# Performance work log

Hardware: AMD Instinct MI355X
Metric: run time of the kernel (lower is better)

The kernel has to match this reference:

```python
import jax, jax.numpy as jnp
import numpy as np

B, S, D, U = 32, 2048, 1024, 1024


def setup_inputs() -> dict:
    key = jax.random.key(0)
    ks = jax.random.split(key, 10)
    s = 0.02
    return {
        "dec_hidden": jax.random.normal(ks[0], (B, D), jnp.float32),
        "enc_output": jax.random.normal(ks[1], (B, S, D), jnp.float32),
        "enc_pad_mask": jnp.ones((B, S), jnp.int32),  # accepted but unused, as in the original
        "use_coverage": True,
        "prev_coverage": jax.random.uniform(ks[2], (B, S, 1), jnp.float32),
        "Ws_w": jax.random.normal(ks[3], (D, U), jnp.float32) * s,
        "Ws_b": jnp.zeros((U,), jnp.float32),
        "Wh_w": jax.random.normal(ks[4], (D, U), jnp.float32) * s,
        "Wh_b": jnp.zeros((U,), jnp.float32),
        "Wc_w": jax.random.normal(ks[5], (1, U), jnp.float32) * s,
        "Wc_b": jnp.zeros((U,), jnp.float32),
        "V_w": jax.random.normal(ks[6], (U, 1), jnp.float32) * s,
        "V_b": jnp.zeros((1,), jnp.float32),
    }


def reference(dec_hidden, enc_output, enc_pad_mask, use_coverage, prev_coverage,
              Ws_w, Ws_b, Wh_w, Wh_b, Wc_w, Wc_b, V_w, V_b):
    # W_h(dec_hidden) with time axis: [B, 1, U]
    h = (dec_hidden @ Wh_w + Wh_b)[:, None, :]
    # W_s(enc_output): [B, S, U]
    feat = jnp.einsum('bsd,du->bsu', enc_output, Ws_w) + Ws_b + h
    if use_coverage and prev_coverage is not None:
        # W_c(prev_coverage): [B, S, 1] @ [1, U] -> [B, S, U]
        feat = feat + prev_coverage @ Wc_w + Wc_b
        score = jnp.tanh(feat) @ V_w + V_b            # [B, S, 1]
        attention_weights = jax.nn.softmax(score, axis=1)
        coverage = attention_weights + prev_coverage
    else:
        score = jnp.tanh(feat) @ V_w + V_b
        attention_weights = jax.nn.softmax(score, axis=1)
        coverage = attention_weights if use_coverage else []
    # weighted sum over sequence axis: [B, D]
    context_vector = jnp.sum(attention_weights * enc_output, axis=1)
    return context_vector, jnp.squeeze(attention_weights, -1), coverage
```

## Files before the change

kernel.cpp:

```cpp
#include <hip/hip_runtime.h>
#include <hip/hip_bf16.h>

namespace {

constexpr int kB = 32;
constexpr int kS = 2048;
constexpr int kD = 1024;
constexpr int kU = 1024;
constexpr int BM = 128;
constexpr int BN = 128;
constexpr int BK = 64;
constexpr int kMT = (kB * kS) / BM;
constexpr int kNT = kU / BN;
constexpr int kKS = kD / BK;
constexpr size_t kChunk = (size_t)BM * BK * 2;

typedef __attribute__((ext_vector_type(8))) short bf16x8;
typedef __attribute__((ext_vector_type(4))) float f32x4;

__device__ __forceinline__ unsigned short f2bf(float x) {
  union { __hip_bfloat16 h; unsigned short u; } c;
  c.h = __float2bfloat16(x);
  return c.u;
}

__device__ __forceinline__ float tanh_fast(float x) {
  float e = __expf(2.0f * x);
  return 1.0f - 2.0f * __builtin_amdgcn_rcpf(e + 1.0f);
}

__device__ __forceinline__ void gload16(const void* g, void* l) {
  __builtin_amdgcn_global_load_lds(
      (const __attribute__((address_space(1))) void*)g,
      (__attribute__((address_space(3))) void*)l, 16, 0, 0);
}


__global__ __launch_bounds__(256) void h2_kernel(
    const float* __restrict__ dec, const float* __restrict__ Whw,
    const float* __restrict__ Whb, const float* __restrict__ Wsb,
    const float* __restrict__ Wcb, float* __restrict__ h2) {
  const int b = blockIdx.y;
  const int u = blockIdx.x * 256 + threadIdx.x;
  float acc = Whb[u] + Wsb[u] + Wcb[u];
  const float* dh = dec + b * kD;
  #pragma unroll 8
  for (int d = 0; d < kD; ++d) acc += dh[d] * Whw[(size_t)d * kU + u];
  h2[b * kU + u] = acc;
}

__global__ __launch_bounds__(256) void context_kernel(
    const float* __restrict__ enc, const float* __restrict__ attn,
    float* __restrict__ ctx) {
  const int b = blockIdx.z;
  const int s0 = blockIdx.y * 256;
  const int d = blockIdx.x * 256 + threadIdx.x;
  const float* e = enc + ((size_t)b * kS + s0) * kD + d;
  const float* a = attn + (size_t)b * kS + s0;
  float acc = 0.f;
  #pragma unroll 8
  for (int s = 0; s < 256; ++s) acc += a[s] * e[(size_t)s * kD];
  atomicAdd(&ctx[b * kD + d], acc);
}


__global__ __launch_bounds__(256) void convA_kernel(
    const float* __restrict__ enc, unsigned char* __restrict__ encT) {
  const size_t e = ((size_t)blockIdx.x * 256 + threadIdx.x) * 8;
  const int r = (int)(e >> 10), d0 = (int)(e & 1023);
  float4 v0 = *(const float4*)(enc + e);
  float4 v1 = *(const float4*)(enc + e + 4);
  uint4 p;
  p.x = (unsigned)f2bf(v0.x) | ((unsigned)f2bf(v0.y) << 16);
  p.y = (unsigned)f2bf(v0.z) | ((unsigned)f2bf(v0.w) << 16);
  p.z = (unsigned)f2bf(v1.x) | ((unsigned)f2bf(v1.y) << 16);
  p.w = (unsigned)f2bf(v1.z) | ((unsigned)f2bf(v1.w) << 16);
  const int mt = r >> 7, row = r & 127, ks = d0 >> 6, c = d0 & 63;
  unsigned char* dst = encT + ((size_t)mt * kKS + ks) * kChunk + row * 128 +
                       (((c >> 3) << 4) ^ ((row & 7) << 4));
  *(uint4*)dst = p;
}

__global__ __launch_bounds__(256) void tpose2_kernel(
    const float* __restrict__ W, unsigned char* __restrict__ Bt) {
  __shared__ float tile[32][33];
  const int u0 = blockIdx.x * 32, d0 = blockIdx.y * 32;
  const int tx = threadIdx.x, ty = threadIdx.y;
  #pragma unroll
  for (int i = 0; i < 4; ++i)
    tile[ty + i * 8][tx] = W[(size_t)(d0 + ty + i * 8) * kU + u0 + tx];
  __syncthreads();
  #pragma unroll
  for (int i = 0; i < 4; ++i) {
    const int u = u0 + ty + i * 8, d = d0 + tx;
    const int nt = u >> 7, n = u & 127, ks = d >> 6, c = d & 63;
    *(unsigned short*)(Bt + ((size_t)nt * kKS + ks) * kChunk + n * 128 +
                       ((((c >> 3) << 4) ^ ((n & 7) << 4)) + (c & 7) * 2)) =
        f2bf(tile[tx][ty + i * 8]);
  }
}

__global__ __launch_bounds__(256, 4) void score_gemm2_kernel(
    const unsigned char* __restrict__ encT, const unsigned char* __restrict__ Bt,
    const float* __restrict__ h2, const float* __restrict__ pc,
    const float* __restrict__ Wcw, const float* __restrict__ Vw,
    float* __restrict__ scorep) {
  __shared__ __attribute__((aligned(16))) unsigned char smA[kChunk];
  __shared__ __attribute__((aligned(16))) unsigned char smB[kChunk];

  const int tid = threadIdx.x;
  const int lane = tid & 63;
  const int w = tid >> 6;
  const int wr = w >> 1, wc = w & 1;

  const int work = (blockIdx.x & 7) * (kMT * kNT / 8) + (blockIdx.x >> 3);
  const int mtile = work >> 3, ntile = work & 7;
  const int r0 = mtile * BM, n0 = ntile * BN;

  const unsigned char* Ab = encT + (size_t)mtile * kKS * kChunk + (size_t)w * 4096 + lane * 16;
  const unsigned char* Bb = Bt + (size_t)ntile * kKS * kChunk + (size_t)w * 4096 + lane * 16;

  f32x4 acc[4][4];
  #pragma unroll
  for (int i = 0; i < 4; ++i)
    #pragma unroll
    for (int j = 0; j < 4; ++j) acc[i][j] = (f32x4){0.f, 0.f, 0.f, 0.f};

  const int lr = lane & 15, lq = lane >> 4;

  for (int ks = 0; ks < kKS; ++ks) {
    #pragma unroll
    for (int i = 0; i < 4; ++i) {
      gload16(Ab + (size_t)ks * kChunk + i * 1024, smA + w * 4096 + i * 1024);
      gload16(Bb + (size_t)ks * kChunk + i * 1024, smB + w * 4096 + i * 1024);
    }
    __syncthreads();
    #pragma unroll
    for (int k2 = 0; k2 < 2; ++k2) {
      const int kb = k2 * 64 + lq * 16;
      bf16x8 af[4], bfr[4];
      #pragma unroll
      for (int fm = 0; fm < 4; ++fm) {
        const int row = wr * 64 + fm * 16 + lr;
        af[fm] = *(const bf16x8*)(smA + row * 128 + (kb ^ ((row & 7) << 4)));
      }
      #pragma unroll
      for (int fn = 0; fn < 4; ++fn) {
        const int n = wc * 64 + fn * 16 + lr;
        bfr[fn] = *(const bf16x8*)(smB + n * 128 + (kb ^ ((n & 7) << 4)));
      }
      #pragma unroll
      for (int fm = 0; fm < 4; ++fm)
        #pragma unroll
        for (int fn = 0; fn < 4; ++fn)
          acc[fm][fn] =
              __builtin_amdgcn_mfma_f32_16x16x32_bf16(af[fm], bfr[fn], acc[fm][fn], 0, 0, 0);
    }
    __syncthreads();
  }

  const int bidx = r0 >> 11;
  float hv[4], wv[4], vv[4];
  #pragma unroll
  for (int fn = 0; fn < 4; ++fn) {
    const int u = n0 + wc * 64 + fn * 16 + lr;
    hv[fn] = h2[bidx * kU + u];
    wv[fn] = Wcw[u];
    vv[fn] = Vw[u];
  }
  float* plane = scorep + (size_t)((ntile << 1) | wc) * (kB * kS);
  #pragma unroll
  for (int fm = 0; fm < 4; ++fm) {
    #pragma unroll
    for (int j = 0; j < 4; ++j) {
      const int r = r0 + wr * 64 + fm * 16 + lq * 4 + j;
      const float pcv = pc[r];
      float partial = 0.f;
      #pragma unroll
      for (int fn = 0; fn < 4; ++fn) {
        const float feat = acc[fm][fn][j] + hv[fn] + pcv * wv[fn];
        partial += tanh_fast(feat) * vv[fn];
      }
      partial += __shfl_xor(partial, 1);
      partial += __shfl_xor(partial, 2);
      partial += __shfl_xor(partial, 4);
      partial += __shfl_xor(partial, 8);
      if (lr == 0) plane[r] = partial;
    }
  }
}

__global__ __launch_bounds__(256) void softmax2_kernel(
    const float* __restrict__ scorep, const float* __restrict__ pc,
    float* __restrict__ attn, float* __restrict__ cov) {
  const int b = blockIdx.x, tid = threadIdx.x;
  const int lane = tid & 63, wid = tid >> 6;
  const size_t base = (size_t)b * kS + tid * 8;
  float v[8] = {0.f, 0.f, 0.f, 0.f, 0.f, 0.f, 0.f, 0.f};
  #pragma unroll
  for (int p = 0; p < 16; ++p) {
    const float* s = scorep + (size_t)p * (kB * kS) + base;
    float4 a = *(const float4*)(s);
    float4 c = *(const float4*)(s + 4);
    v[0] += a.x; v[1] += a.y; v[2] += a.z; v[3] += a.w;
    v[4] += c.x; v[5] += c.y; v[6] += c.z; v[7] += c.w;
  }
  float m = v[0];
  #pragma unroll
  for (int i = 1; i < 8; ++i) m = fmaxf(m, v[i]);
  #pragma unroll
  for (int msk = 1; msk < 64; msk <<= 1) m = fmaxf(m, __shfl_xor(m, msk));
  __shared__ float redm[4], reds[4];
  if (lane == 0) redm[wid] = m;
  __syncthreads();
  m = fmaxf(fmaxf(redm[0], redm[1]), fmaxf(redm[2], redm[3]));
  float e[8], sum = 0.f;
  #pragma unroll
  for (int i = 0; i < 8; ++i) { e[i] = __expf(v[i] - m); sum += e[i]; }
  #pragma unroll
  for (int msk = 1; msk < 64; msk <<= 1) sum += __shfl_xor(sum, msk);
  if (lane == 0) reds[wid] = sum;
  __syncthreads();
  sum = reds[0] + reds[1] + reds[2] + reds[3];
  const float inv = 1.0f / sum;
  float pv[8], a[8], c[8];
  const float* p = pc + base;
  *(float4*)(pv) = *(const float4*)(p);
  *(float4*)(pv + 4) = *(const float4*)(p + 4);
  #pragma unroll
  for (int i = 0; i < 8; ++i) { a[i] = e[i] * inv; c[i] = a[i] + pv[i]; }
  *(float4*)(attn + base) = *(float4*)(a);
  *(float4*)(attn + base + 4) = *(float4*)(a + 4);
  *(float4*)(cov + base) = *(float4*)(c);
  *(float4*)(cov + base + 4) = *(float4*)(c + 4);
}


__global__ __launch_bounds__(256) void tpose_fb_kernel(
    const float* __restrict__ W, unsigned short* __restrict__ out) {
  __shared__ float tile[32][33];
  const int u0 = blockIdx.x * 32, d0 = blockIdx.y * 32;
  const int tx = threadIdx.x, ty = threadIdx.y;
  #pragma unroll
  for (int i = 0; i < 4; ++i)
    tile[ty + i * 8][tx] = W[(size_t)(d0 + ty + i * 8) * kU + u0 + tx];
  __syncthreads();
  #pragma unroll
  for (int i = 0; i < 4; ++i)
    out[(size_t)(u0 + ty + i * 8) * kD + d0 + tx] = f2bf(tile[tx][ty + i * 8]);
}

__global__ __launch_bounds__(256, 2) void score_gemm_fb_kernel(
    const float* __restrict__ enc, const unsigned short* __restrict__ WsT,
    const float* __restrict__ h2, const float* __restrict__ pc,
    const float* __restrict__ Wcw, const float* __restrict__ Vw,
    float* __restrict__ score) {
  __shared__ __attribute__((aligned(16))) unsigned char smA[BM * BK * 2];
  __shared__ __attribute__((aligned(16))) unsigned char smB[BN * BK * 2];
  const int tid = threadIdx.x;
  const int lane = tid & 63;
  const int wid = tid >> 6;
  const int wr = wid >> 1, wc = wid & 1;
  const int mtile = blockIdx.x >> 3, ntile = blockIdx.x & 7;
  const int r0 = mtile * BM, n0 = ntile * BN;
  f32x4 acc[4][4];
  #pragma unroll
  for (int i = 0; i < 4; ++i)
    #pragma unroll
    for (int j = 0; j < 4; ++j) acc[i][j] = (f32x4){0.f, 0.f, 0.f, 0.f};
  const int kqA = tid & 15;
  const int rowA = tid >> 4;
  const int kcB = tid & 7;
  const int nB = tid >> 3;
  float4 aReg[8];
  uint4 bReg[4];
  #pragma unroll
  for (int i = 0; i < 8; ++i)
    aReg[i] = *(const float4*)(enc + (size_t)(r0 + rowA + 16 * i) * kD + kqA * 4);
  #pragma unroll
  for (int i = 0; i < 4; ++i)
    bReg[i] = *(const uint4*)(WsT + (size_t)(n0 + nB + 32 * i) * kD + kcB * 8);
  const int lr = lane & 15, lq = lane >> 4;
  for (int k0 = 0; k0 < kD; k0 += BK) {
    #pragma unroll
    for (int i = 0; i < 8; ++i) {
      const int row = rowA + 16 * i;
      uint2 p;
      p.x = (unsigned)f2bf(aReg[i].x) | ((unsigned)f2bf(aReg[i].y) << 16);
      p.y = (unsigned)f2bf(aReg[i].z) | ((unsigned)f2bf(aReg[i].w) << 16);
      *(uint2*)(smA + row * 128 + ((kqA * 8) ^ ((row & 7) << 4))) = p;
    }
    #pragma unroll
    for (int i = 0; i < 4; ++i) {
      const int n = nB + 32 * i;
      *(uint4*)(smB + n * 128 + ((kcB * 16) ^ ((n & 7) << 4))) = bReg[i];
    }
    __syncthreads();
    if (k0 + BK < kD) {
      const int kn = k0 + BK;
      #pragma unroll
      for (int i = 0; i < 8; ++i)
        aReg[i] = *(const float4*)(enc + (size_t)(r0 + rowA + 16 * i) * kD + kn + kqA * 4);
      #pragma unroll
      for (int i = 0; i < 4; ++i)
        bReg[i] = *(const uint4*)(WsT + (size_t)(n0 + nB + 32 * i) * kD + kn + kcB * 8);
    }
    #pragma unroll
    for (int ks = 0; ks < 2; ++ks) {
      const int kb = ks * 64 + lq * 16;
      bf16x8 af[4], bfr[4];
      #pragma unroll
      for (int fm = 0; fm < 4; ++fm) {
        const int row = wr * 64 + fm * 16 + lr;
        af[fm] = *(const bf16x8*)(smA + row * 128 + (kb ^ ((row & 7) << 4)));
      }
      #pragma unroll
      for (int fn = 0; fn < 4; ++fn) {
        const int n = wc * 64 + fn * 16 + lr;
        bfr[fn] = *(const bf16x8*)(smB + n * 128 + (kb ^ ((n & 7) << 4)));
      }
      #pragma unroll
      for (int fm = 0; fm < 4; ++fm)
        #pragma unroll
        for (int fn = 0; fn < 4; ++fn)
          acc[fm][fn] =
              __builtin_amdgcn_mfma_f32_16x16x32_bf16(af[fm], bfr[fn], acc[fm][fn], 0, 0, 0);
    }
    __syncthreads();
  }
  const int bidx = r0 >> 11;
  float hv[4], wv[4], vv[4];
  #pragma unroll
  for (int fn = 0; fn < 4; ++fn) {
    const int u = n0 + wc * 64 + fn * 16 + lr;
    hv[fn] = h2[bidx * kU + u];
    wv[fn] = Wcw[u];
    vv[fn] = Vw[u];
  }
  #pragma unroll
  for (int fm = 0; fm < 4; ++fm) {
    #pragma unroll
    for (int j = 0; j < 4; ++j) {
      const int r = r0 + wr * 64 + fm * 16 + lq * 4 + j;
      const float pcv = pc[r];
      float partial = 0.f;
      #pragma unroll
      for (int fn = 0; fn < 4; ++fn) {
        const float feat = acc[fm][fn][j] + hv[fn] + pcv * wv[fn];
        partial += tanh_fast(feat) * vv[fn];
      }
      partial += __shfl_xor(partial, 1);
      partial += __shfl_xor(partial, 2);
      partial += __shfl_xor(partial, 4);
      partial += __shfl_xor(partial, 8);
      if (lr == 0) atomicAdd(&score[r], partial);
    }
  }
}

__global__ __launch_bounds__(256) void softmax_fb_kernel(
    const float* __restrict__ score, const float* __restrict__ pc,
    float* __restrict__ attn, float* __restrict__ cov) {
  const int b = blockIdx.x, tid = threadIdx.x;
  const int lane = tid & 63, wid = tid >> 6;
  const float* s = score + (size_t)b * kS;
  float v[8];
  *(float4*)(v) = *(const float4*)(s + tid * 8);
  *(float4*)(v + 4) = *(const float4*)(s + tid * 8 + 4);
  float m = v[0];
  #pragma unroll
  for (int i = 1; i < 8; ++i) m = fmaxf(m, v[i]);
  #pragma unroll
  for (int msk = 1; msk < 64; msk <<= 1) m = fmaxf(m, __shfl_xor(m, msk));
  __shared__ float redm[4], reds[4];
  if (lane == 0) redm[wid] = m;
  __syncthreads();
  m = fmaxf(fmaxf(redm[0], redm[1]), fmaxf(redm[2], redm[3]));
  float e[8], sum = 0.f;
  #pragma unroll
  for (int i = 0; i < 8; ++i) { e[i] = __expf(v[i] - m); sum += e[i]; }
  #pragma unroll
  for (int msk = 1; msk < 64; msk <<= 1) sum += __shfl_xor(sum, msk);
  if (lane == 0) reds[wid] = sum;
  __syncthreads();
  sum = reds[0] + reds[1] + reds[2] + reds[3];
  const float inv = 1.0f / sum;
  float pv[8], a[8], c[8];
  const float* p = pc + (size_t)b * kS + tid * 8;
  *(float4*)(pv) = *(const float4*)(p);
  *(float4*)(pv + 4) = *(const float4*)(p + 4);
  #pragma unroll
  for (int i = 0; i < 8; ++i) { a[i] = e[i] * inv; c[i] = a[i] + pv[i]; }
  *(float4*)(attn + (size_t)b * kS + tid * 8) = *(float4*)(a);
  *(float4*)(attn + (size_t)b * kS + tid * 8 + 4) = *(float4*)(a + 4);
  *(float4*)(cov + (size_t)b * kS + tid * 8) = *(float4*)(c);
  *(float4*)(cov + (size_t)b * kS + tid * 8 + 4) = *(float4*)(c + 4);
}

}

extern "C" void kernel_launch(void* const* d_in, const int* in_sizes, int n_in,
                              void* d_out, int out_size, void* d_ws, size_t ws_size,
                              hipStream_t stream) {
  (void)in_sizes; (void)n_in; (void)out_size;
  const float* dec = (const float*)d_in[0];
  const float* enc = (const float*)d_in[1];
  const float* pc  = (const float*)d_in[4];
  const float* Wsw = (const float*)d_in[5];
  const float* Wsb = (const float*)d_in[6];
  const float* Whw = (const float*)d_in[7];
  const float* Whb = (const float*)d_in[8];
  const float* Wcw = (const float*)d_in[9];
  const float* Wcb = (const float*)d_in[10];
  const float* Vw  = (const float*)d_in[11];

  float* ctx  = (float*)d_out;
  float* attn = (float*)d_out + kB * kD;
  float* cov  = attn + kB * kS;

  unsigned char* ws = (unsigned char*)d_ws;

  const size_t encT_sz  = (size_t)kB * kS * kD * 2;
  const size_t Bt_sz    = (size_t)kU * kD * 2;
  const size_t h2_sz    = (size_t)kB * kU * 4;
  const size_t sp_sz    = (size_t)16 * kB * kS * 4;
  const size_t need     = encT_sz + Bt_sz + h2_sz + sp_sz;

  hipMemsetAsync(ctx, 0, kB * kD * sizeof(float), stream);

  if (ws_size >= need) {
    unsigned char* encT = ws;
    unsigned char* Bt   = ws + encT_sz;
    float* h2     = (float*)(ws + encT_sz + Bt_sz);
    float* scorep = (float*)(ws + encT_sz + Bt_sz + h2_sz);

    convA_kernel<<<dim3((kB * kS * kD / 8) / 256), 256, 0, stream>>>(enc, encT);
    tpose2_kernel<<<dim3(kU / 32, kD / 32), dim3(32, 8), 0, stream>>>(Wsw, Bt);
    h2_kernel<<<dim3(kU / 256, kB), 256, 0, stream>>>(dec, Whw, Whb, Wsb, Wcb, h2);
    score_gemm2_kernel<<<dim3(kMT * kNT), 256, 0, stream>>>(
        encT, Bt, h2, pc, Wcw, Vw, scorep);
    softmax2_kernel<<<dim3(kB), 256, 0, stream>>>(scorep, pc, attn, cov);
    context_kernel<<<dim3(kD / 256, kS / 256, kB), 256, 0, stream>>>(enc, attn, ctx);
  } else {
    unsigned short* WsT = (unsigned short*)ws;
    float* h2    = (float*)(ws + (size_t)2 * 1024 * 1024);
    float* score = (float*)(ws + (size_t)2 * 1024 * 1024 + 131072);
    hipMemsetAsync(score, 0, kB * kS * sizeof(float), stream);
    h2_kernel<<<dim3(kU / 256, kB), 256, 0, stream>>>(dec, Whw, Whb, Wsb, Wcb, h2);
    tpose_fb_kernel<<<dim3(kU / 32, kD / 32), dim3(32, 8), 0, stream>>>(Wsw, WsT);
    score_gemm_fb_kernel<<<dim3(kMT * kNT), 256, 0, stream>>>(
        enc, WsT, h2, pc, Wcw, Vw, score);
    softmax_fb_kernel<<<dim3(kB), 256, 0, stream>>>(score, pc, attn, cov);
    context_kernel<<<dim3(kD / 256, kS / 256, kB), 256, 0, stream>>>(enc, attn, ctx);
  }
}
```

Baseline: 347.0 us.

## Fuse prep kernels and compute context from bf16 encoder copy

```diff
diff --git a/kernel.cpp b/kernel.cpp
--- a/kernel.cpp
+++ b/kernel.cpp
@@ -7,13 +7,16 @@
 constexpr int kS = 2048;
 constexpr int kD = 1024;
 constexpr int kU = 1024;
-constexpr int BM = 128;
-constexpr int BN = 128;
-constexpr int BK = 64;
-constexpr int kMT = (kB * kS) / BM;
-constexpr int kNT = kU / BN;
-constexpr int kKS = kD / BK;
-constexpr size_t kChunk = (size_t)BM * BK * 2;
+
+constexpr int kKT = kD / 64;
+constexpr size_t kHalf = 16384;
+constexpr size_t kTileChunk = 2 * kHalf;
+constexpr size_t kPanel = (size_t)kKT * kTileChunk;
+
+constexpr int kConvBlocks = (kB * kS * kD / 8) / 256;
+constexpr int kTpBlocks = (kU / 32) * (kD / 32);
+constexpr int kH2Blocks = (kU / 64) * (kB / 4);
+constexpr int kPrepBlocks = kConvBlocks + kTpBlocks + kH2Blocks;
 
 typedef __attribute__((ext_vector_type(8))) short bf16x8;
 typedef __attribute__((ext_vector_type(4))) float f32x4;
@@ -24,6 +27,12 @@
   return c.u;
 }
 
+__device__ __forceinline__ float bf2f(unsigned short u) {
+  union { unsigned int i; float f; } c;
+  c.i = ((unsigned int)u) << 16;
+  return c.f;
+}
+
 __device__ __forceinline__ float tanh_fast(float x) {
   float e = __expf(2.0f * x);
   return 1.0f - 2.0f * __builtin_amdgcn_rcpf(e + 1.0f);
@@ -35,21 +44,419 @@
       (__attribute__((address_space(3))) void*)l, 16, 0, 0);
 }
 
-
-__global__ __launch_bounds__(256) void h2_kernel(
+#define MFMA_BF16(a, b, c) __builtin_amdgcn_mfma_f32_16x16x32_bf16((a), (b), (c), 0, 0, 0)
+
+
+__global__ __launch_bounds__(256) void prep_kernel(
+    const float* __restrict__ enc, unsigned char* __restrict__ encT,
+    const float* __restrict__ Wsw, unsigned char* __restrict__ Bt,
     const float* __restrict__ dec, const float* __restrict__ Whw,
     const float* __restrict__ Whb, const float* __restrict__ Wsb,
     const float* __restrict__ Wcb, float* __restrict__ h2) {
+  __shared__ float tile[32][33];
+  const int bid = blockIdx.x;
+  if (bid < kConvBlocks) {
+    const size_t e = ((size_t)bid * 256 + threadIdx.x) * 8;
+    const int r = (int)(e >> 10), d0 = (int)(e & 1023);
+    float4 v0 = *(const float4*)(enc + e);
+    float4 v1 = *(const float4*)(enc + e + 4);
+    uint4 p;
+    p.x = (unsigned)f2bf(v0.x) | ((unsigned)f2bf(v0.y) << 16);
+    p.y = (unsigned)f2bf(v0.z) | ((unsigned)f2bf(v0.w) << 16);
+    p.z = (unsigned)f2bf(v1.x) | ((unsigned)f2bf(v1.y) << 16);
+    p.w = (unsigned)f2bf(v1.z) | ((unsigned)f2bf(v1.w) << 16);
+    const int mt = r >> 8, rh = (r >> 7) & 1, row = r & 127;
+    const int kt = d0 >> 6, c8 = (d0 & 63) >> 3;
+    unsigned char* dst = encT + (size_t)mt * kPanel + (size_t)kt * kTileChunk +
+                         (size_t)rh * kHalf + row * 128 +
+                         (((unsigned)c8 << 4) ^ (((unsigned)row & 7) << 4));
+    *(uint4*)dst = p;
+  } else if (bid < kConvBlocks + kTpBlocks) {
+    const int q = bid - kConvBlocks;
+    const int u0 = (q & 31) * 32, d0 = (q >> 5) * 32;
+    const int tx = threadIdx.x & 31, ty = threadIdx.x >> 5;
+    #pragma unroll
+    for (int i = 0; i < 4; ++i)
+      tile[ty + i * 8][tx] = Wsw[(size_t)(d0 + ty + i * 8) * kU + u0 + tx];
+    __syncthreads();
+    #pragma unroll
+    for (int i = 0; i < 4; ++i) {
+      const int u = u0 + ty + i * 8, d = d0 + tx;
+      const int nt = u >> 8, gh = (u >> 7) & 1, n = u & 127;
+      const int kt = d >> 6, c = d & 63;
+      *(unsigned short*)(Bt + (size_t)nt * kPanel + (size_t)kt * kTileChunk +
+                         (size_t)gh * kHalf + n * 128 +
+                         (((((unsigned)c >> 3) << 4) ^ (((unsigned)n & 7) << 4)) +
+                          (c & 7) * 2)) = f2bf(tile[tx][ty + i * 8]);
+    }
+  } else {
+    const int q = bid - kConvBlocks - kTpBlocks;
+    const int u = (q & 15) * 64 + (threadIdx.x & 63);
+    const int b = (q >> 4) * 4 + (threadIdx.x >> 6);
+    float acc = 0.f;
+    const float* dh = dec + b * kD;
+    #pragma unroll 8
+    for (int d = 0; d < kD; ++d) acc += dh[d] * Whw[(size_t)d * kU + u];
+    h2[b * kU + u] = acc + Whb[u] + Wsb[u] + Wcb[u];
+  }
+}
+
+__global__ __launch_bounds__(256, 8) void score_gemm6_kernel(
+    const unsigned char* __restrict__ encT, const unsigned char* __restrict__ Bt,
+    const float* __restrict__ h2, const float* __restrict__ pc,
+    const float* __restrict__ Wcw, const float* __restrict__ Vw,
+    float* __restrict__ scorep) {
+  __shared__ __attribute__((aligned(16))) unsigned char smA[16384];
+  __shared__ __attribute__((aligned(16))) unsigned char smB[16384];
+
+  const int tid = threadIdx.x;
+  const int lane = tid & 63;
+  const int w = tid >> 6;
+  const int wr = w >> 1, wc = w & 1;
+  const int work = (blockIdx.x & 7) * 512 + (blockIdx.x >> 3);
+  const int mtile = work >> 3, ntile = work & 7;
+  const int r0 = mtile * 128, n0 = ntile * 128;
+
+  const unsigned char* Ab = encT + (size_t)(mtile >> 1) * kPanel +
+                            (size_t)(mtile & 1) * kHalf + (size_t)w * 4096 + lane * 16;
+  const unsigned char* Bb = Bt + (size_t)(ntile >> 1) * kPanel +
+                            (size_t)(ntile & 1) * kHalf + (size_t)w * 4096 + lane * 16;
+
+  f32x4 acc[4][4];
+  #pragma unroll
+  for (int i = 0; i < 4; ++i)
+    #pragma unroll
+    for (int j = 0; j < 4; ++j) acc[i][j] = (f32x4){0.f, 0.f, 0.f, 0.f};
+
+  const int lr = lane & 15, lq = lane >> 4;
+
+  for (int ks = 0; ks < kKT; ++ks) {
+    #pragma unroll
+    for (int i = 0; i < 4; ++i) {
+      gload16(Ab + (size_t)ks * kTileChunk + i * 1024, smA + w * 4096 + i * 1024);
+      gload16(Bb + (size_t)ks * kTileChunk + i * 1024, smB + w * 4096 + i * 1024);
+    }
+    __syncthreads();
+    #pragma unroll
+    for (int k2 = 0; k2 < 2; ++k2) {
+      const int kb = k2 * 64 + lq * 16;
+      bf16x8 af[4], bfr[4];
+      #pragma unroll
+      for (int fm = 0; fm < 4; ++fm) {
+        const int row = wr * 64 + fm * 16 + lr;
+        af[fm] = *(const bf16x8*)(smA + row * 128 + (kb ^ ((row & 7) << 4)));
+      }
+      #pragma unroll
+      for (int fn = 0; fn < 4; ++fn) {
+        const int n = wc * 64 + fn * 16 + lr;
+        bfr[fn] = *(const bf16x8*)(smB + n * 128 + (kb ^ ((n & 7) << 4)));
+      }
+      #pragma unroll
+      for (int fm = 0; fm < 4; ++fm)
+        #pragma unroll
+        for (int fn = 0; fn < 4; ++fn)
+          acc[fm][fn] = MFMA_BF16(af[fm], bfr[fn], acc[fm][fn]);
+    }
+    __syncthreads();
+  }
+
+  const int bidx = r0 >> 11;
+  float hv[4], wv[4], vv[4];
+  #pragma unroll
+  for (int fn = 0; fn < 4; ++fn) {
+    const int u = n0 + wc * 64 + fn * 16 + lr;
+    hv[fn] = h2[bidx * kU + u];
+    wv[fn] = Wcw[u];
+    vv[fn] = Vw[u];
+  }
+  float* plane = scorep + (size_t)((ntile << 1) | wc) * (kB * kS);
+  #pragma unroll
+  for (int fm = 0; fm < 4; ++fm) {
+    #pragma unroll
+    for (int j = 0; j < 4; ++j) {
+      const int r = r0 + wr * 64 + fm * 16 + lq * 4 + j;
+      const float pcv = pc[r];
+      float partial = 0.f;
+      #pragma unroll
+      for (int fn = 0; fn < 4; ++fn) {
+        const float feat = acc[fm][fn][j] + hv[fn] + pcv * wv[fn];
+        partial += tanh_fast(feat) * vv[fn];
+      }
+      partial += __shfl_xor(partial, 1);
+      partial += __shfl_xor(partial, 2);
+      partial += __shfl_xor(partial, 4);
+      partial += __shfl_xor(partial, 8);
+      if (lr == 0) plane[r] = partial;
+    }
+  }
+}
+
+__global__ __launch_bounds__(256) void softmax2_kernel(
+    const float* __restrict__ scorep, const float* __restrict__ pc,
+    float* __restrict__ attn, float* __restrict__ cov) {
+  const int b = blockIdx.x, tid = threadIdx.x;
+  const int lane = tid & 63, wid = tid >> 6;
+  const size_t base = (size_t)b * kS + tid * 8;
+  float v[8] = {0.f, 0.f, 0.f, 0.f, 0.f, 0.f, 0.f, 0.f};
+  #pragma unroll
+  for (int p = 0; p < 16; ++p) {
+    const float* s = scorep + (size_t)p * (kB * kS) + base;
+    float4 a = *(const float4*)(s);
+    float4 c = *(const float4*)(s + 4);
+    v[0] += a.x; v[1] += a.y; v[2] += a.z; v[3] += a.w;
+    v[4] += c.x; v[5] += c.y; v[6] += c.z; v[7] += c.w;
+  }
+  float m = v[0];
+  #pragma unroll
+  for (int i = 1; i < 8; ++i) m = fmaxf(m, v[i]);
+  #pragma unroll
+  for (int msk = 1; msk < 64; msk <<= 1) m = fmaxf(m, __shfl_xor(m, msk));
+  __shared__ float redm[4], reds[4];
+  if (lane == 0) redm[wid] = m;
+  __syncthreads();
+  m = fmaxf(fmaxf(redm[0], redm[1]), fmaxf(redm[2], redm[3]));
+  float e[8], sum = 0.f;
+  #pragma unroll
+  for (int i = 0; i < 8; ++i) { e[i] = __expf(v[i] - m); sum += e[i]; }
+  #pragma unroll
+  for (int msk = 1; msk < 64; msk <<= 1) sum += __shfl_xor(sum, msk);
+  if (lane == 0) reds[wid] = sum;
+  __syncthreads();
+  sum = reds[0] + reds[1] + reds[2] + reds[3];
+  const float inv = 1.0f / sum;
+  float pv[8], a[8], c[8];
+  const float* p = pc + base;
+  *(float4*)(pv) = *(const float4*)(p);
+  *(float4*)(pv + 4) = *(const float4*)(p + 4);
+  #pragma unroll
+  for (int i = 0; i < 8; ++i) { a[i] = e[i] * inv; c[i] = a[i] + pv[i]; }
+  *(float4*)(attn + base) = *(float4*)(a);
+  *(float4*)(attn + base + 4) = *(float4*)(a + 4);
+  *(float4*)(cov + base) = *(float4*)(c);
+  *(float4*)(cov + base + 4) = *(float4*)(c + 4);
+}
+
+__global__ __launch_bounds__(256) void context2_kernel(
+    const unsigned char* __restrict__ encT, const float* __restrict__ attn,
+    float* __restrict__ ctx) {
+  const int kt = blockIdx.x;
   const int b = blockIdx.y;
-  const int u = blockIdx.x * 256 + threadIdx.x;
-  float acc = Whb[u] + Wsb[u] + Wcb[u];
+  const int cg = threadIdx.x & 7;
+  const int rgrp = threadIdx.x >> 3;
+  float acc8[8];
+  #pragma unroll
+  for (int j = 0; j < 8; ++j) acc8[j] = 0.f;
+  const float* ab = attn + (size_t)b * kS;
+  for (int it = 0; it < kS / 32; ++it) {
+    const int s = it * 32 + rgrp;
+    const int r = b * kS + s;
+    const int mt = r >> 8, rh = (r >> 7) & 1, row = r & 127;
+    const unsigned char* chunk = encT + (size_t)mt * kPanel +
+                                 (size_t)kt * kTileChunk + (size_t)rh * kHalf;
+    uint4 v = *(const uint4*)(chunk + row * 128 +
+                              ((((unsigned)cg << 4) ^ (((unsigned)row & 7) << 4))));
+    const float a = ab[s];
+    const unsigned int* vw = (const unsigned int*)&v;
+    #pragma unroll
+    for (int q = 0; q < 4; ++q) {
+      acc8[2 * q]     += a * bf2f((unsigned short)(vw[q] & 0xffff));
+      acc8[2 * q + 1] += a * bf2f((unsigned short)(vw[q] >> 16));
+    }
+  }
+  __shared__ float red[256 * 8];
+  #pragma unroll
+  for (int j = 0; j < 8; ++j) red[threadIdx.x * 8 + j] = acc8[j];
+  __syncthreads();
+  for (int stride = 16; stride > 0; stride >>= 1) {
+    if (rgrp < stride) {
+      #pragma unroll
+      for (int j = 0; j < 8; ++j)
+        red[(rgrp * 8 + cg) * 8 + j] += red[((rgrp + stride) * 8 + cg) * 8 + j];
+    }
+    __syncthreads();
+  }
+  if (rgrp == 0) {
+    #pragma unroll
+    for (int j = 0; j < 8; ++j)
+      ctx[(size_t)b * kD + kt * 64 + cg * 8 + j] = red[cg * 8 + j];
+  }
+}
+
+
+__global__ __launch_bounds__(256) void h2b_kernel(
+    const float* __restrict__ dec, const float* __restrict__ Whw,
+    const float* __restrict__ Whb, const float* __restrict__ Wsb,
+    const float* __restrict__ Wcb, float* __restrict__ h2) {
+  const int u = blockIdx.x * 64 + (threadIdx.x & 63);
+  const int b = blockIdx.y * 4 + (threadIdx.x >> 6);
+  float acc = 0.f;
   const float* dh = dec + b * kD;
   #pragma unroll 8
   for (int d = 0; d < kD; ++d) acc += dh[d] * Whw[(size_t)d * kU + u];
-  h2[b * kU + u] = acc;
-}
-
-__global__ __launch_bounds__(256) void context_kernel(
+  h2[b * kU + u] = acc + Whb[u] + Wsb[u] + Wcb[u];
+}
+
+__global__ __launch_bounds__(256) void tpose_fb_kernel(
+    const float* __restrict__ W, unsigned short* __restrict__ out) {
+  __shared__ float tile[32][33];
+  const int u0 = blockIdx.x * 32, d0 = blockIdx.y * 32;
+  const int tx = threadIdx.x & 31, ty = threadIdx.x >> 5;
+  #pragma unroll
+  for (int i = 0; i < 4; ++i)
+    tile[ty + i * 8][tx] = W[(size_t)(d0 + ty + i * 8) * kU + u0 + tx];
+  __syncthreads();
+  #pragma unroll
+  for (int i = 0; i < 4; ++i)
+    out[(size_t)(u0 + ty + i * 8) * kD + d0 + tx] = f2bf(tile[tx][ty + i * 8]);
+}
+
+__global__ __launch_bounds__(256, 2) void score_gemm_fb_kernel(
+    const float* __restrict__ enc, const unsigned short* __restrict__ WsT,
+    const float* __restrict__ h2, const float* __restrict__ pc,
+    const float* __restrict__ Wcw, const float* __restrict__ Vw,
+    float* __restrict__ score) {
+  __shared__ __attribute__((aligned(16))) unsigned char smA[128 * 64 * 2];
+  __shared__ __attribute__((aligned(16))) unsigned char smB[128 * 64 * 2];
+  const int tid = threadIdx.x;
+  const int lane = tid & 63;
+  const int wid = tid >> 6;
+  const int wr = wid >> 1, wc = wid & 1;
+  const int mtile = blockIdx.x >> 3, ntile = blockIdx.x & 7;
+  const int r0 = mtile * 128, n0 = ntile * 128;
+  f32x4 acc[4][4];
+  #pragma unroll
+  for (int i = 0; i < 4; ++i)
+    #pragma unroll
+    for (int j = 0; j < 4; ++j) acc[i][j] = (f32x4){0.f, 0.f, 0.f, 0.f};
+  const int kqA = tid & 15;
+  const int rowA = tid >> 4;
+  const int kcB = tid & 7;
+  const int nB = tid >> 3;
+  float4 aReg[8];
+  uint4 bReg[4];
+  #pragma unroll
+  for (int i = 0; i < 8; ++i)
+    aReg[i] = *(const float4*)(enc + (size_t)(r0 + rowA + 16 * i) * kD + kqA * 4);
+  #pragma unroll
+  for (int i = 0; i < 4; ++i)
+    bReg[i] = *(const uint4*)(WsT + (size_t)(n0 + nB + 32 * i) * kD + kcB * 8);
+  const int lr = lane & 15, lq = lane >> 4;
+  for (int k0 = 0; k0 < kD; k0 += 64) {
+    #pragma unroll
+    for (int i = 0; i < 8; ++i) {
+      const int row = rowA + 16 * i;
+      uint2 p;
+      p.x = (unsigned)f2bf(aReg[i].x) | ((unsigned)f2bf(aReg[i].y) << 16);
+      p.y = (unsigned)f2bf(aReg[i].z) | ((unsigned)f2bf(aReg[i].w) << 16);
+      *(uint2*)(smA + row * 128 + ((kqA * 8) ^ ((row & 7) << 4))) = p;
+    }
+    #pragma unroll
+    for (int i = 0; i < 4; ++i) {
+      const int n = nB + 32 * i;
+      *(uint4*)(smB + n * 128 + ((kcB * 16) ^ ((n & 7) << 4))) = bReg[i];
+    }
+    __syncthreads();
+    if (k0 + 64 < kD) {
+      const int kn = k0 + 64;
+      #pragma unroll
+      for (int i = 0; i < 8; ++i)
+        aReg[i] = *(const float4*)(enc + (size_t)(r0 + rowA + 16 * i) * kD + kn + kqA * 4);
+      #pragma unroll
+      for (int i = 0; i < 4; ++i)
+        bReg[i] = *(const uint4*)(WsT + (size_t)(n0 + nB + 32 * i) * kD + kn + kcB * 8);
+    }
+    #pragma unroll
+    for (int ks = 0; ks < 2; ++ks) {
+      const int kb = ks * 64 + lq * 16;
+      bf16x8 af2[4], bfr[4];
+      #pragma unroll
+      for (int fm = 0; fm < 4; ++fm) {
+        const int row = wr * 64 + fm * 16 + lr;
+        af2[fm] = *(const bf16x8*)(smA + row * 128 + (kb ^ ((row & 7) << 4)));
+      }
+      #pragma unroll
+      for (int fn = 0; fn < 4; ++fn) {
+        const int n = wc * 64 + fn * 16 + lr;
+        bfr[fn] = *(const bf16x8*)(smB + n * 128 + (kb ^ ((n & 7) << 4)));
+      }
+      #pragma unroll
+      for (int fm = 0; fm < 4; ++fm)
+        #pragma unroll
+        for (int fn = 0; fn < 4; ++fn)
+          acc[fm][fn] = MFMA_BF16(af2[fm], bfr[fn], acc[fm][fn]);
+    }
+    __syncthreads();
+  }
+  const int bidx = r0 >> 11;
+  float hv[4], wv[4], vv[4];
+  #pragma unroll
+  for (int fn = 0; fn < 4; ++fn) {
+    const int u = n0 + wc * 64 + fn * 16 + lr;
+    hv[fn] = h2[bidx * kU + u];
+    wv[fn] = Wcw[u];
+    vv[fn] = Vw[u];
+  }
+  #pragma unroll
+  for (int fm = 0; fm < 4; ++fm) {
+    #pragma unroll
+    for (int j = 0; j < 4; ++j) {
+      const int r = r0 + wr * 64 + fm * 16 + lq * 4 + j;
+      const float pcv = pc[r];
+      float partial = 0.f;
+      #pragma unroll
+      for (int fn = 0; fn < 4; ++fn) {
+        const float feat = acc[fm][fn][j] + hv[fn] + pcv * wv[fn];
+        partial += tanh_fast(feat) * vv[fn];
+      }
+      partial += __shfl_xor(partial, 1);
+      partial += __shfl_xor(partial, 2);
+      partial += __shfl_xor(partial, 4);
+      partial += __shfl_xor(partial, 8);
+      if (lr == 0) atomicAdd(&score[r], partial);
+    }
+  }
+}
+
+__global__ __launch_bounds__(256) void softmax_fb_kernel(
+    const float* __restrict__ score, const float* __restrict__ pc,
+    float* __restrict__ attn, float* __restrict__ cov) {
+  const int b = blockIdx.x, tid = threadIdx.x;
+  const int lane = tid & 63, wid = tid >> 6;
+  const float* s = score + (size_t)b * kS;
+  float v[8];
+  *(float4*)(v) = *(const float4*)(s + tid * 8);
+  *(float4*)(v + 4) = *(const float4*)(s + tid * 8 + 4);
+  float m = v[0];
+  #pragma unroll
+  for (int i = 1; i < 8; ++i) m = fmaxf(m, v[i]);
+  #pragma unroll
+  for (int msk = 1; msk < 64; msk <<= 1) m = fmaxf(m, __shfl_xor(m, msk));
+  __shared__ float redm[4], reds[4];
+  if (lane == 0) redm[wid] = m;
+  __syncthreads();
+  m = fmaxf(fmaxf(redm[0], redm[1]), fmaxf(redm[2], redm[3]));
+  float e[8], sum = 0.f;
+  #pragma unroll
+  for (int i = 0; i < 8; ++i) { e[i] = __expf(v[i] - m); sum += e[i]; }
+  #pragma unroll
+  for (int msk = 1; msk < 64; msk <<= 1) sum += __shfl_xor(sum, msk);
+  if (lane == 0) reds[wid] = sum;
+  __syncthreads();
+  sum = reds[0] + reds[1] + reds[2] + reds[3];
+  const float inv = 1.0f / sum;
+  float pv[8], a[8], c[8];
+  const float* p = pc + (size_t)b * kS + tid * 8;
+  *(float4*)(pv) = *(const float4*)(p);
+  *(float4*)(pv + 4) = *(const float4*)(p + 4);
+  #pragma unroll
+  for (int i = 0; i < 8; ++i) { a[i] = e[i] * inv; c[i] = a[i] + pv[i]; }
+  *(float4*)(attn + (size_t)b * kS + tid * 8) = *(float4*)(a);
+  *(float4*)(attn + (size_t)b * kS + tid * 8 + 4) = *(float4*)(a + 4);
+  *(float4*)(cov + (size_t)b * kS + tid * 8) = *(float4*)(c);
+  *(float4*)(cov + (size_t)b * kS + tid * 8 + 4) = *(float4*)(c + 4);
+}
+
+__global__ __launch_bounds__(256) void context_fb_kernel(
     const float* __restrict__ enc, const float* __restrict__ attn,
     float* __restrict__ ctx) {
   const int b = blockIdx.z;
@@ -61,340 +468,6 @@
   #pragma unroll 8
   for (int s = 0; s < 256; ++s) acc += a[s] * e[(size_t)s * kD];
   atomicAdd(&ctx[b * kD + d], acc);
-}
-
-
-__global__ __launch_bounds__(256) void convA_kernel(
-    const float* __restrict__ enc, unsigned char* __restrict__ encT) {
-  const size_t e = ((size_t)blockIdx.x * 256 + threadIdx.x) * 8;
-  const int r = (int)(e >> 10), d0 = (int)(e & 1023);
-  float4 v0 = *(const float4*)(enc + e);
-  float4 v1 = *(const float4*)(enc + e + 4);
-  uint4 p;
-  p.x = (unsigned)f2bf(v0.x) | ((unsigned)f2bf(v0.y) << 16);
-  p.y = (unsigned)f2bf(v0.z) | ((unsigned)f2bf(v0.w) << 16);
-  p.z = (unsigned)f2bf(v1.x) | ((unsigned)f2bf(v1.y) << 16);
-  p.w = (unsigned)f2bf(v1.z) | ((unsigned)f2bf(v1.w) << 16);
-  const int mt = r >> 7, row = r & 127, ks = d0 >> 6, c = d0 & 63;
-  unsigned char* dst = encT + ((size_t)mt * kKS + ks) * kChunk + row * 128 +
-                       (((c >> 3) << 4) ^ ((row & 7) << 4));
-  *(uint4*)dst = p;
-}
-
-__global__ __launch_bounds__(256) void tpose2_kernel(
-    const float* __restrict__ W, unsigned char* __restrict__ Bt) {
-  __shared__ float tile[32][33];
-  const int u0 = blockIdx.x * 32, d0 = blockIdx.y * 32;
-  const int tx = threadIdx.x, ty = threadIdx.y;
-  #pragma unroll
-  for (int i = 0; i < 4; ++i)
-    tile[ty + i * 8][tx] = W[(size_t)(d0 + ty + i * 8) * kU + u0 + tx];
-  __syncthreads();
-  #pragma unroll
-  for (int i = 0; i < 4; ++i) {
-    const int u = u0 + ty + i * 8, d = d0 + tx;
-    const int nt = u >> 7, n = u & 127, ks = d >> 6, c = d & 63;
-    *(unsigned short*)(Bt + ((size_t)nt * kKS + ks) * kChunk + n * 128 +
-                       ((((c >> 3) << 4) ^ ((n & 7) << 4)) + (c & 7) * 2)) =
-        f2bf(tile[tx][ty + i * 8]);
-  }
-}
-
-__global__ __launch_bounds__(256, 4) void score_gemm2_kernel(
-    const unsigned char* __restrict__ encT, const unsigned char* __restrict__ Bt,
-    const float* __restrict__ h2, const float* __restrict__ pc,
-    const float* __restrict__ Wcw, const float* __restrict__ Vw,
-    float* __restrict__ scorep) {
-  __shared__ __attribute__((aligned(16))) unsigned char smA[kChunk];
-  __shared__ __attribute__((aligned(16))) unsigned char smB[kChunk];
-
-  const int tid = threadIdx.x;
-  const int lane = tid & 63;
-  const int w = tid >> 6;
-  const int wr = w >> 1, wc = w & 1;
-
-  const int work = (blockIdx.x & 7) * (kMT * kNT / 8) + (blockIdx.x >> 3);
-  const int mtile = work >> 3, ntile = work & 7;
-  const int r0 = mtile * BM, n0 = ntile * BN;
-
-  const unsigned char* Ab = encT + (size_t)mtile * kKS * kChunk + (size_t)w * 4096 + lane * 16;
-  const unsigned char* Bb = Bt + (size_t)ntile * kKS * kChunk + (size_t)w * 4096 + lane * 16;
-
-  f32x4 acc[4][4];
-  #pragma unroll
-  for (int i = 0; i < 4; ++i)
-    #pragma unroll
-    for (int j = 0; j < 4; ++j) acc[i][j] = (f32x4){0.f, 0.f, 0.f, 0.f};
-
-  const int lr = lane & 15, lq = lane >> 4;
-
-  for (int ks = 0; ks < kKS; ++ks) {
-    #pragma unroll
-    for (int i = 0; i < 4; ++i) {
-      gload16(Ab + (size_t)ks * kChunk + i * 1024, smA + w * 4096 + i * 1024);
-      gload16(Bb + (size_t)ks * kChunk + i * 1024, smB + w * 4096 + i * 1024);
-    }
-    __syncthreads();
-    #pragma unroll
-    for (int k2 = 0; k2 < 2; ++k2) {
-      const int kb = k2 * 64 + lq * 16;
-      bf16x8 af[4], bfr[4];
-      #pragma unroll
-      for (int fm = 0; fm < 4; ++fm) {
-        const int row = wr * 64 + fm * 16 + lr;
-        af[fm] = *(const bf16x8*)(smA + row * 128 + (kb ^ ((row & 7) << 4)));
-      }
-      #pragma unroll
-      for (int fn = 0; fn < 4; ++fn) {
-        const int n = wc * 64 + fn * 16 + lr;
-        bfr[fn] = *(const bf16x8*)(smB + n * 128 + (kb ^ ((n & 7) << 4)));
-      }
-      #pragma unroll
-      for (int fm = 0; fm < 4; ++fm)
-        #pragma unroll
-        for (int fn = 0; fn < 4; ++fn)
-          acc[fm][fn] =
-              __builtin_amdgcn_mfma_f32_16x16x32_bf16(af[fm], bfr[fn], acc[fm][fn], 0, 0, 0);
-    }
-    __syncthreads();
-  }
-
-  const int bidx = r0 >> 11;
-  float hv[4], wv[4], vv[4];
-  #pragma unroll
-  for (int fn = 0; fn < 4; ++fn) {
-    const int u = n0 + wc * 64 + fn * 16 + lr;
-    hv[fn] = h2[bidx * kU + u];
-    wv[fn] = Wcw[u];
-    vv[fn] = Vw[u];
-  }
-  float* plane = scorep + (size_t)((ntile << 1) | wc) * (kB * kS);
-  #pragma unroll
-  for (int fm = 0; fm < 4; ++fm) {
-    #pragma unroll
-    for (int j = 0; j < 4; ++j) {
-      const int r = r0 + wr * 64 + fm * 16 + lq * 4 + j;
-      const float pcv = pc[r];
-      float partial = 0.f;
-      #pragma unroll
-      for (int fn = 0; fn < 4; ++fn) {
-        const float feat = acc[fm][fn][j] + hv[fn] + pcv * wv[fn];
-        partial += tanh_fast(feat) * vv[fn];
-      }
-      partial += __shfl_xor(partial, 1);
-      partial += __shfl_xor(partial, 2);
-      partial += __shfl_xor(partial, 4);
-      partial += __shfl_xor(partial, 8);
-      if (lr == 0) plane[r] = partial;
-    }
-  }
-}
-
-__global__ __launch_bounds__(256) void softmax2_kernel(
-    const float* __restrict__ scorep, const float* __restrict__ pc,
-    float* __restrict__ attn, float* __restrict__ cov) {
-  const int b = blockIdx.x, tid = threadIdx.x;
-  const int lane = tid & 63, wid = tid >> 6;
-  const size_t base = (size_t)b * kS + tid * 8;
-  float v[8] = {0.f, 0.f, 0.f, 0.f, 0.f, 0.f, 0.f, 0.f};
-  #pragma unroll
-  for (int p = 0; p < 16; ++p) {
-    const float* s = scorep + (size_t)p * (kB * kS) + base;
-    float4 a = *(const float4*)(s);
-    float4 c = *(const float4*)(s + 4);
-    v[0] += a.x; v[1] += a.y; v[2] += a.z; v[3] += a.w;
-    v[4] += c.x; v[5] += c.y; v[6] += c.z; v[7] += c.w;
-  }
-  float m = v[0];
-  #pragma unroll
-  for (int i = 1; i < 8; ++i) m = fmaxf(m, v[i]);
-  #pragma unroll
-  for (int msk = 1; msk < 64; msk <<= 1) m = fmaxf(m, __shfl_xor(m, msk));
-  __shared__ float redm[4], reds[4];
-  if (lane == 0) redm[wid] = m;
-  __syncthreads();
-  m = fmaxf(fmaxf(redm[0], redm[1]), fmaxf(redm[2], redm[3]));
-  float e[8], sum = 0.f;
-  #pragma unroll
-  for (int i = 0; i < 8; ++i) { e[i] = __expf(v[i] - m); sum += e[i]; }
-  #pragma unroll
-  for (int msk = 1; msk < 64; msk <<= 1) sum += __shfl_xor(sum, msk);
-  if (lane == 0) reds[wid] = sum;
-  __syncthreads();
-  sum = reds[0] + reds[1] + reds[2] + reds[3];
-  const float inv = 1.0f / sum;
-  float pv[8], a[8], c[8];
-  const float* p = pc + base;
-  *(float4*)(pv) = *(const float4*)(p);
-  *(float4*)(pv + 4) = *(const float4*)(p + 4);
-  #pragma unroll
-  for (int i = 0; i < 8; ++i) { a[i] = e[i] * inv; c[i] = a[i] + pv[i]; }
-  *(float4*)(attn + base) = *(float4*)(a);
-  *(float4*)(attn + base + 4) = *(float4*)(a + 4);
-  *(float4*)(cov + base) = *(float4*)(c);
-  *(float4*)(cov + base + 4) = *(float4*)(c + 4);
-}
-
-
-__global__ __launch_bounds__(256) void tpose_fb_kernel(
-    const float* __restrict__ W, unsigned short* __restrict__ out) {
-  __shared__ float tile[32][33];
-  const int u0 = blockIdx.x * 32, d0 = blockIdx.y * 32;
-  const int tx = threadIdx.x, ty = threadIdx.y;
-  #pragma unroll
-  for (int i = 0; i < 4; ++i)
-    tile[ty + i * 8][tx] = W[(size_t)(d0 + ty + i * 8) * kU + u0 + tx];
-  __syncthreads();
-  #pragma unroll
-  for (int i = 0; i < 4; ++i)
-    out[(size_t)(u0 + ty + i * 8) * kD + d0 + tx] = f2bf(tile[tx][ty + i * 8]);
-}
-
-__global__ __launch_bounds__(256, 2) void score_gemm_fb_kernel(
-    const float* __restrict__ enc, const unsigned short* __restrict__ WsT,
-    const float* __restrict__ h2, const float* __restrict__ pc,
-    const float* __restrict__ Wcw, const float* __restrict__ Vw,
-    float* __restrict__ score) {
-  __shared__ __attribute__((aligned(16))) unsigned char smA[BM * BK * 2];
-  __shared__ __attribute__((aligned(16))) unsigned char smB[BN * BK * 2];
-  const int tid = threadIdx.x;
-  const int lane = tid & 63;
-  const int wid = tid >> 6;
-  const int wr = wid >> 1, wc = wid & 1;
-  const int mtile = blockIdx.x >> 3, ntile = blockIdx.x & 7;
-  const int r0 = mtile * BM, n0 = ntile * BN;
-  f32x4 acc[4][4];
-  #pragma unroll
-  for (int i = 0; i < 4; ++i)
-    #pragma unroll
-    for (int j = 0; j < 4; ++j) acc[i][j] = (f32x4){0.f, 0.f, 0.f, 0.f};
-  const int kqA = tid & 15;
-  const int rowA = tid >> 4;
-  const int kcB = tid & 7;
-  const int nB = tid >> 3;
-  float4 aReg[8];
-  uint4 bReg[4];
-  #pragma unroll
-  for (int i = 0; i < 8; ++i)
-    aReg[i] = *(const float4*)(enc + (size_t)(r0 + rowA + 16 * i) * kD + kqA * 4);
-  #pragma unroll
-  for (int i = 0; i < 4; ++i)
-    bReg[i] = *(const uint4*)(WsT + (size_t)(n0 + nB + 32 * i) * kD + kcB * 8);
-  const int lr = lane & 15, lq = lane >> 4;
-  for (int k0 = 0; k0 < kD; k0 += BK) {
-    #pragma unroll
-    for (int i = 0; i < 8; ++i) {
-      const int row = rowA + 16 * i;
-      uint2 p;
-      p.x = (unsigned)f2bf(aReg[i].x) | ((unsigned)f2bf(aReg[i].y) << 16);
-      p.y = (unsigned)f2bf(aReg[i].z) | ((unsigned)f2bf(aReg[i].w) << 16);
-      *(uint2*)(smA + row * 128 + ((kqA * 8) ^ ((row & 7) << 4))) = p;
-    }
-    #pragma unroll
-    for (int i = 0; i < 4; ++i) {
-      const int n = nB + 32 * i;
-      *(uint4*)(smB + n * 128 + ((kcB * 16) ^ ((n & 7) << 4))) = bReg[i];
-    }
-    __syncthreads();
-    if (k0 + BK < kD) {
-      const int kn = k0 + BK;
-      #pragma unroll
-      for (int i = 0; i < 8; ++i)
-        aReg[i] = *(const float4*)(enc + (size_t)(r0 + rowA + 16 * i) * kD + kn + kqA * 4);
-      #pragma unroll
-      for (int i = 0; i < 4; ++i)
-        bReg[i] = *(const uint4*)(WsT + (size_t)(n0 + nB + 32 * i) * kD + kn + kcB * 8);
-    }
-    #pragma unroll
-    for (int ks = 0; ks < 2; ++ks) {
-      const int kb = ks * 64 + lq * 16;
-      bf16x8 af[4], bfr[4];
-      #pragma unroll
-      for (int fm = 0; fm < 4; ++fm) {
-        const int row = wr * 64 + fm * 16 + lr;
-        af[fm] = *(const bf16x8*)(smA + row * 128 + (kb ^ ((row & 7) << 4)));
-      }
-      #pragma unroll
-      for (int fn = 0; fn < 4; ++fn) {
-        const int n = wc * 64 + fn * 16 + lr;
-        bfr[fn] = *(const bf16x8*)(smB + n * 128 + (kb ^ ((n & 7) << 4)));
-      }
-      #pragma unroll
-      for (int fm = 0; fm < 4; ++fm)
-        #pragma unroll
-        for (int fn = 0; fn < 4; ++fn)
-          acc[fm][fn] =
-              __builtin_amdgcn_mfma_f32_16x16x32_bf16(af[fm], bfr[fn], acc[fm][fn], 0, 0, 0);
-    }
-    __syncthreads();
-  }
-  const int bidx = r0 >> 11;
-  float hv[4], wv[4], vv[4];
-  #pragma unroll
-  for (int fn = 0; fn < 4; ++fn) {
-    const int u = n0 + wc * 64 + fn * 16 + lr;
-    hv[fn] = h2[bidx * kU + u];
-    wv[fn] = Wcw[u];
-    vv[fn] = Vw[u];
-  }
-  #pragma unroll
-  for (int fm = 0; fm < 4; ++fm) {
-    #pragma unroll
-    for (int j = 0; j < 4; ++j) {
-      const int r = r0 + wr * 64 + fm * 16 + lq * 4 + j;
-      const float pcv = pc[r];
-      float partial = 0.f;
-      #pragma unroll
-      for (int fn = 0; fn < 4; ++fn) {
-        const float feat = acc[fm][fn][j] + hv[fn] + pcv * wv[fn];
-        partial += tanh_fast(feat) * vv[fn];
-      }
-      partial += __shfl_xor(partial, 1);
-      partial += __shfl_xor(partial, 2);
-      partial += __shfl_xor(partial, 4);
-      partial += __shfl_xor(partial, 8);
-      if (lr == 0) atomicAdd(&score[r], partial);
-    }
-  }
-}
-
-__global__ __launch_bounds__(256) void softmax_fb_kernel(
-    const float* __restrict__ score, const float* __restrict__ pc,
-    float* __restrict__ attn, float* __restrict__ cov) {
-  const int b = blockIdx.x, tid = threadIdx.x;
-  const int lane = tid & 63, wid = tid >> 6;
-  const float* s = score + (size_t)b * kS;
-  float v[8];
-  *(float4*)(v) = *(const float4*)(s + tid * 8);
-  *(float4*)(v + 4) = *(const float4*)(s + tid * 8 + 4);
-  float m = v[0];
-  #pragma unroll
-  for (int i = 1; i < 8; ++i) m = fmaxf(m, v[i]);
-  #pragma unroll
-  for (int msk = 1; msk < 64; msk <<= 1) m = fmaxf(m, __shfl_xor(m, msk));
-  __shared__ float redm[4], reds[4];
-  if (lane == 0) redm[wid] = m;
-  __syncthreads();
-  m = fmaxf(fmaxf(redm[0], redm[1]), fmaxf(redm[2], redm[3]));
-  float e[8], sum = 0.f;
-  #pragma unroll
-  for (int i = 0; i < 8; ++i) { e[i] = __expf(v[i] - m); sum += e[i]; }
-  #pragma unroll
-  for (int msk = 1; msk < 64; msk <<= 1) sum += __shfl_xor(sum, msk);
-  if (lane == 0) reds[wid] = sum;
-  __syncthreads();
-  sum = reds[0] + reds[1] + reds[2] + reds[3];
-  const float inv = 1.0f / sum;
-  float pv[8], a[8], c[8];
-  const float* p = pc + (size_t)b * kS + tid * 8;
-  *(float4*)(pv) = *(const float4*)(p);
-  *(float4*)(pv + 4) = *(const float4*)(p + 4);
-  #pragma unroll
-  for (int i = 0; i < 8; ++i) { a[i] = e[i] * inv; c[i] = a[i] + pv[i]; }
-  *(float4*)(attn + (size_t)b * kS + tid * 8) = *(float4*)(a);
-  *(float4*)(attn + (size_t)b * kS + tid * 8 + 4) = *(float4*)(a + 4);
-  *(float4*)(cov + (size_t)b * kS + tid * 8) = *(float4*)(c);
-  *(float4*)(cov + (size_t)b * kS + tid * 8 + 4) = *(float4*)(c + 4);
 }
 
 }
@@ -420,13 +493,11 @@
 
   unsigned char* ws = (unsigned char*)d_ws;
 
-  const size_t encT_sz  = (size_t)kB * kS * kD * 2;
-  const size_t Bt_sz    = (size_t)kU * kD * 2;
-  const size_t h2_sz    = (size_t)kB * kU * 4;
-  const size_t sp_sz    = (size_t)16 * kB * kS * 4;
-  const size_t need     = encT_sz + Bt_sz + h2_sz + sp_sz;
-
-  hipMemsetAsync(ctx, 0, kB * kD * sizeof(float), stream);
+  const size_t encT_sz = (size_t)kB * kS * kD * 2;
+  const size_t Bt_sz   = (size_t)kU * kD * 2;
+  const size_t h2_sz   = (size_t)kB * kU * 4;
+  const size_t sp_sz   = (size_t)16 * kB * kS * 4;
+  const size_t need    = encT_sz + Bt_sz + h2_sz + sp_sz;
 
   if (ws_size >= need) {
     unsigned char* encT = ws;
@@ -434,23 +505,23 @@
     float* h2     = (float*)(ws + encT_sz + Bt_sz);
     float* scorep = (float*)(ws + encT_sz + Bt_sz + h2_sz);
 
-    convA_kernel<<<dim3((kB * kS * kD / 8) / 256), 256, 0, stream>>>(enc, encT);
-    tpose2_kernel<<<dim3(kU / 32, kD / 32), dim3(32, 8), 0, stream>>>(Wsw, Bt);
-    h2_kernel<<<dim3(kU / 256, kB), 256, 0, stream>>>(dec, Whw, Whb, Wsb, Wcb, h2);
-    score_gemm2_kernel<<<dim3(kMT * kNT), 256, 0, stream>>>(
+    prep_kernel<<<dim3(kPrepBlocks), 256, 0, stream>>>(
+        enc, encT, Wsw, Bt, dec, Whw, Whb, Wsb, Wcb, h2);
+    score_gemm6_kernel<<<dim3(4096), 256, 0, stream>>>(
         encT, Bt, h2, pc, Wcw, Vw, scorep);
     softmax2_kernel<<<dim3(kB), 256, 0, stream>>>(scorep, pc, attn, cov);
-    context_kernel<<<dim3(kD / 256, kS / 256, kB), 256, 0, stream>>>(enc, attn, ctx);
+    context2_kernel<<<dim3(kD / 64, kB), 256, 0, stream>>>(encT, attn, ctx);
   } else {
     unsigned short* WsT = (unsigned short*)ws;
     float* h2    = (float*)(ws + (size_t)2 * 1024 * 1024);
     float* score = (float*)(ws + (size_t)2 * 1024 * 1024 + 131072);
     hipMemsetAsync(score, 0, kB * kS * sizeof(float), stream);
-    h2_kernel<<<dim3(kU / 256, kB), 256, 0, stream>>>(dec, Whw, Whb, Wsb, Wcb, h2);
-    tpose_fb_kernel<<<dim3(kU / 32, kD / 32), dim3(32, 8), 0, stream>>>(Wsw, WsT);
-    score_gemm_fb_kernel<<<dim3(kMT * kNT), 256, 0, stream>>>(
+    hipMemsetAsync(ctx, 0, kB * kD * sizeof(float), stream);
+    h2b_kernel<<<dim3(kU / 64, kB / 4), 256, 0, stream>>>(dec, Whw, Whb, Wsb, Wcb, h2);
+    tpose_fb_kernel<<<dim3(kU / 32, kD / 32), 256, 0, stream>>>(Wsw, WsT);
+    score_gemm_fb_kernel<<<dim3(4096), 256, 0, stream>>>(
         enc, WsT, h2, pc, Wcw, Vw, score);
     softmax_fb_kernel<<<dim3(kB), 256, 0, stream>>>(score, pc, attn, cov);
-    context_kernel<<<dim3(kD / 256, kS / 256, kB), 256, 0, stream>>>(enc, attn, ctx);
-  }
-}
+    context_fb_kernel<<<dim3(kD / 256, kS / 256, kB), 256, 0, stream>>>(enc, attn, ctx);
+  }
+}
```

Result: slower. 380.3 us (+9.6%).
